# Performance work log

Measured on AMD Instinct MI355X. Metric: run time of the kernel, lower is better.

Reference implementation:

```python
import jax, jax.numpy as jnp
import numpy as np

H_DIM = 1024
NUM_HEADS = 16
HEAD_DIM = H_DIM // NUM_HEADS
EPS = 1e-5


def rms_norm(x, w, eps=EPS):
    var = jnp.mean(jnp.square(x), axis=-1, keepdims=True)
    return x * jax.lax.rsqrt(var + eps) * w


def setup_inputs() -> dict:
    key = jax.random.key(0)
    ks = jax.random.split(key, 8)
    B, S = 2, 2048
    x = jax.random.normal(ks[0], (B, S, H_DIM), dtype=jnp.float32)
    # learned params (orthogonal init approximated by scaled normal for a correctness baseline)
    qkv_w = jax.random.normal(ks[1], (3 * H_DIM, H_DIM), dtype=jnp.float32) / np.sqrt(H_DIM)
    gate_w = jax.random.normal(ks[2], (NUM_HEADS, H_DIM), dtype=jnp.float32) / np.sqrt(H_DIM)
    o_w = jax.random.normal(ks[3], (H_DIM, H_DIM), dtype=jnp.float32) / np.sqrt(H_DIM)
    prenorm_w = jnp.ones((H_DIM,), dtype=jnp.float32)
    q_norm_w = jnp.ones((HEAD_DIM,), dtype=jnp.float32)
    k_norm_w = jnp.ones((HEAD_DIM,), dtype=jnp.float32)
    return {"x": x, "prenorm_w": prenorm_w, "qkv_w": qkv_w, "gate_w": gate_w,
            "o_w": o_w, "q_norm_w": q_norm_w, "k_norm_w": k_norm_w}


def reference(x, prenorm_w, qkv_w, gate_w, o_w, q_norm_w, k_norm_w):
    B, S, D = x.shape
    residual = x
    xn = rms_norm(x, prenorm_w)                                   # [B,S,D]
    qkv = jnp.einsum('bsd,ed->bse', xn, qkv_w)                    # [B,S,3D]
    qkv = qkv.reshape(B, S, 3, NUM_HEADS, HEAD_DIM)
    gate = jnp.einsum('bsd,hd->bsh', xn, gate_w)                  # [B,S,H]
    q, k, v = qkv[:, :, 0], qkv[:, :, 1], qkv[:, :, 2]            # [B,S,H,hd]
    q = rms_norm(q, q_norm_w)
    k = rms_norm(k, k_norm_w)
    scale = 1.0 / np.sqrt(HEAD_DIM).astype(np.float32)
    scores = jnp.einsum('bqhd,bkhd->bhqk', q, k) * scale          # [B,H,S,S]
    attn = jax.nn.softmax(scores, axis=-1)
    out = jnp.einsum('bhqk,bkhd->bhqd', attn, v)                  # [B,H,S,hd]
    out = out * jax.nn.sigmoid(gate).transpose(0, 2, 1)[..., None]
    out = out.transpose(0, 2, 1, 3).reshape(B, S, D)              # [B,S,D]
    return jnp.einsum('bsd,ed->bse', out, o_w) + residual
```

## Files before the change

kernel.cpp:

```cpp
#include <hip/hip_runtime.h>
#include <math.h>

typedef __bf16 bf16x8 __attribute__((ext_vector_type(8)));
typedef float f32x4 __attribute__((ext_vector_type(4)));
typedef float f32x16 __attribute__((ext_vector_type(16)));
typedef unsigned int uint2v __attribute__((ext_vector_type(2)));
typedef unsigned int uint4v __attribute__((ext_vector_type(4)));
typedef unsigned short ushort_t;

#define SEQ 2048
#define MROWS 4096
#define EPS 1e-5f
#define QKS 3200
#define LOG2E 1.4426950408889634f
#define SMAX_B2 17.32f

__device__ __forceinline__ float bf2f(ushort_t u) {
  union { unsigned int i; float f; } c; c.i = ((unsigned int)u) << 16; return c.f;
}
__device__ __forceinline__ ushort_t f2bf(float f) {
  union { unsigned int i; float f; } c; c.f = f;
  unsigned int i = c.i;
  unsigned int r = i + 0x7fffu + ((i >> 16) & 1u);
  return (ushort_t)(r >> 16);
}
__device__ __forceinline__ ushort_t f2bf_fast(float f) {
  union { __bf16 b; ushort_t u; } cv; cv.b = (__bf16)f; return cv.u;
}

__device__ __forceinline__ float exp2_raw(float x) {
  float r; asm("v_exp_f32 %0, %1" : "=v"(r) : "v"(x)); return r;
}

#define CVTPK(d, a, b) asm("v_cvt_pk_bf16_f32 %0, %1, %2" : "=v"(d) : "v"(a), "v"(b))

__device__ __forceinline__ void plane_swap(unsigned int &a, unsigned int &b) {
#if __has_builtin(__builtin_amdgcn_permlane32_swap)
  uint2v r = __builtin_amdgcn_permlane32_swap(a, b, 0, 0);
  a = r.x; b = r.y;
#else
  unsigned int sa = (unsigned int)__shfl_xor((int)a, 32);
  unsigned int sb = (unsigned int)__shfl_xor((int)b, 32);
  int hi = (int)((threadIdx.x & 63) >> 5);
  unsigned int na = hi ? sb : a;
  unsigned int nb = hi ? b : sa;
  a = na; b = nb;
#endif
}

__device__ __forceinline__ void softmax_pack(const f32x16 &stv, float &lp,
                                             uint4v &Fa, uint4v &Fb) {
  float p[16];
  #pragma unroll
  for (int r = 0; r < 16; ++r) p[r] = exp2_raw(stv[r] - SMAX_B2);
  float s0 = (p[0] + p[1]) + (p[2] + p[3]);
  float s1 = (p[4] + p[5]) + (p[6] + p[7]);
  float s2 = (p[8] + p[9]) + (p[10] + p[11]);
  float s3 = (p[12] + p[13]) + (p[14] + p[15]);
  lp += (s0 + s1) + (s2 + s3);
  unsigned int X00, X01, X10, X11, X20, X21, X30, X31;
  CVTPK(X00, p[0], p[1]);   CVTPK(X01, p[2], p[3]);
  CVTPK(X10, p[4], p[5]);   CVTPK(X11, p[6], p[7]);
  CVTPK(X20, p[8], p[9]);   CVTPK(X21, p[10], p[11]);
  CVTPK(X30, p[12], p[13]); CVTPK(X31, p[14], p[15]);
  plane_swap(X00, X10); plane_swap(X01, X11);
  plane_swap(X20, X30); plane_swap(X21, X31);
  Fa.x = X00; Fa.y = X01; Fa.z = X10; Fa.w = X11;
  Fb.x = X20; Fb.y = X21; Fb.z = X30; Fb.w = X31;
}

__device__ __forceinline__ float wave_sum(float v) {
  #pragma unroll
  for (int off = 32; off > 0; off >>= 1) v += __shfl_xor(v, off);
  return v;
}

__global__ void detect_kernel(const unsigned int* __restrict__ xraw, int* __restrict__ flag) {
  int tid = threadIdx.x;
  int cnt = 0;
  for (int i = tid; i < 4096; i += 256) {
    unsigned int e = (xraw[i] >> 7) & 0xFFu;
    cnt += (e >= 100u && e <= 150u) ? 1 : 0;
  }
  __shared__ int sred[256];
  sred[tid] = cnt;
  __syncthreads();
  for (int s = 128; s > 0; s >>= 1) {
    if (tid < s) sred[tid] += sred[tid + s];
    __syncthreads();
  }
  if (tid == 0) flag[0] = (sred[0] > 2048) ? 1 : 0;
}

__global__ void prep_kernel(const void* __restrict__ qkvw_in, const void* __restrict__ gw_in,
                            const void* __restrict__ ow_in, const void* __restrict__ pw_in,
                            const void* __restrict__ qn_in, const void* __restrict__ kn_in,
                            ushort_t* __restrict__ Wcat, ushort_t* __restrict__ ow,
                            float* __restrict__ pwf, float* __restrict__ qnf,
                            float* __restrict__ knf, const int* __restrict__ flag) {
  int bid = blockIdx.x, tid = threadIdx.x;
  int bf = *flag;
  if (bid < 12288) {
    int i = bid * 256 + tid;
    Wcat[i] = bf ? ((const ushort_t*)qkvw_in)[i] : f2bf(((const float*)qkvw_in)[i]);
  } else if (bid < 12352) {
    int i = (bid - 12288) * 256 + tid;
    Wcat[3072 * 1024 + i] = bf ? ((const ushort_t*)gw_in)[i] : f2bf(((const float*)gw_in)[i]);
  } else if (bid < 16448) {
    int i = (bid - 12352) * 256 + tid;
    ow[i] = bf ? ((const ushort_t*)ow_in)[i] : f2bf(((const float*)ow_in)[i]);
  } else {
    for (int i = tid; i < 1024; i += 256)
      pwf[i] = bf ? bf2f(((const ushort_t*)pw_in)[i]) : ((const float*)pw_in)[i];
    if (tid < 64) {
      qnf[tid] = bf ? bf2f(((const ushort_t*)qn_in)[tid]) : ((const float*)qn_in)[tid];
      knf[tid] = bf ? bf2f(((const ushort_t*)kn_in)[tid]) : ((const float*)kn_in)[tid];
    }
  }
}

__global__ void prenorm_kernel(const void* __restrict__ xraw,
                               const float* __restrict__ w,
                               ushort_t* __restrict__ xn,
                               const int* __restrict__ flag) {
  int row = blockIdx.x;
  int tid = threadIdx.x;
  float4 u;
  if (*flag) {
    ushort4 s = ((const ushort4*)xraw)[row * 256 + tid];
    u.x = bf2f(s.x); u.y = bf2f(s.y); u.z = bf2f(s.z); u.w = bf2f(s.w);
  } else {
    u = ((const float4*)xraw)[row * 256 + tid];
  }
  float ss = u.x*u.x + u.y*u.y + u.z*u.z + u.w*u.w;
  ss = wave_sum(ss);
  __shared__ float red[4];
  if ((tid & 63) == 0) red[tid >> 6] = ss;
  __syncthreads();
  float total = red[0] + red[1] + red[2] + red[3];
  float inv = rsqrtf(total * (1.0f / 1024.0f) + EPS);
  float4 wu = ((const float4*)w)[tid];
  ushort4 o;
  o.x = f2bf(u.x * inv * wu.x);
  o.y = f2bf(u.y * inv * wu.y);
  o.z = f2bf(u.z * inv * wu.z);
  o.w = f2bf(u.w * inv * wu.w);
  ((ushort4*)(xn + (long long)row * 1024))[tid] = o;
}

__device__ __forceinline__ void gll16(const ushort_t* g, ushort_t* l) {
  __builtin_amdgcn_global_load_lds(
      (const __attribute__((address_space(1))) unsigned int*)g,
      (__attribute__((address_space(3))) unsigned int*)l, 16, 0, 0);
}

__global__ void gemm_qkv_fused(const ushort_t* __restrict__ A, const ushort_t* __restrict__ B,
                               ushort_t* __restrict__ C, float* __restrict__ gate,
                               const float* __restrict__ qw, const float* __restrict__ kw) {
  __shared__ ushort_t As[128 * 32];
  __shared__ ushort_t Bs[128 * 32];
  int tid = threadIdx.x, wave = tid >> 6, lane = tid & 63;
  int m_blk = blockIdx.y * 128, n_blk = blockIdx.x * 128;
  int wm = (wave & 1) * 64, wn = (wave >> 1) * 64;
  int g = lane >> 4, c = lane & 15;
  int arow = lane >> 2;
  int akc = (lane & 3) << 3;
  f32x4 acc[4][4] = {};
  for (int kt = 0; kt < 1024; kt += 32) {
    #pragma unroll
    for (int i = 0; i < 2; ++i) {
      int rbase = (i * 4 + wave) * 16;
      gll16(A + (long long)(m_blk + rbase + arow) * 1024 + kt + akc, &As[rbase * 32]);
      gll16(B + (long long)(n_blk + rbase + arow) * 1024 + kt + akc, &Bs[rbase * 32]);
    }
    __syncthreads();
    bf16x8 af[4], bfr[4];
    #pragma unroll
    for (int mi = 0; mi < 4; ++mi)
      af[mi] = *(const bf16x8*)&As[(wm + mi * 16 + c) * 32 + (g << 3)];
    #pragma unroll
    for (int ni = 0; ni < 4; ++ni)
      bfr[ni] = *(const bf16x8*)&Bs[(wn + ni * 16 + c) * 32 + (g << 3)];
    #pragma unroll
    for (int mi = 0; mi < 4; ++mi)
      #pragma unroll
      for (int ni = 0; ni < 4; ++ni)
        acc[mi][ni] = __builtin_amdgcn_mfma_f32_16x16x32_bf16(af[mi], bfr[ni], acc[mi][ni], 0, 0, 0);
    __syncthreads();
  }
  int col_base = n_blk + wn;
  if (col_base < 2048) {
    int isk = col_base >= 1024;
    float scale = isk ? 1.0f : (0.125f * LOG2E);
    const float* nw = isk ? kw : qw;
    float w[4];
    #pragma unroll
    for (int ni = 0; ni < 4; ++ni) w[ni] = nw[ni * 16 + c];
    #pragma unroll
    for (int mi = 0; mi < 4; ++mi)
      #pragma unroll
      for (int r = 0; r < 4; ++r) {
        float ss = 0.f;
        #pragma unroll
        for (int ni = 0; ni < 4; ++ni) ss += acc[mi][ni][r] * acc[mi][ni][r];
        #pragma unroll
        for (int off = 8; off > 0; off >>= 1) ss += __shfl_xor(ss, off);
        float inv = rsqrtf(ss * (1.0f / 64.0f) + EPS) * scale;
        int row = m_blk + wm + mi * 16 + g * 4 + r;
        #pragma unroll
        for (int ni = 0; ni < 4; ++ni)
          C[(long long)row * QKS + col_base + ni * 16 + c] = f2bf(acc[mi][ni][r] * inv * w[ni]);
      }
  } else if (col_base < 3072) {
    #pragma unroll
    for (int mi = 0; mi < 4; ++mi)
      #pragma unroll
      for (int r = 0; r < 4; ++r) {
        int row = m_blk + wm + mi * 16 + g * 4 + r;
        #pragma unroll
        for (int ni = 0; ni < 4; ++ni)
          C[(long long)row * QKS + col_base + ni * 16 + c] = f2bf(acc[mi][ni][r]);
      }
  } else if (col_base == 3072) {
    #pragma unroll
    for (int mi = 0; mi < 4; ++mi)
      #pragma unroll
      for (int r = 0; r < 4; ++r) {
        int row = m_blk + wm + mi * 16 + g * 4 + r;
        float v = acc[mi][0][r];
        gate[(long long)row * 16 + c] = 1.0f / (1.0f + __expf(-v));
      }
  }
}

__global__ void gemm_tiled(const ushort_t* __restrict__ A, const ushort_t* __restrict__ B,
                           void* __restrict__ Cv, const void* __restrict__ res,
                           const int* __restrict__ flag,
                           int K, int lda, int ldb, int ldc) {
  __shared__ ushort_t As[128 * 32];
  __shared__ ushort_t Bs[128 * 32];
  int tid = threadIdx.x, wave = tid >> 6, lane = tid & 63;
  int m_blk = blockIdx.y * 128, n_blk = blockIdx.x * 128;
  int wm = (wave & 1) * 64, wn = (wave >> 1) * 64;
  int g = lane >> 4, c = lane & 15;
  int arow = lane >> 2;
  int akc = (lane & 3) << 3;
  f32x4 acc[4][4] = {};
  for (int kt = 0; kt < K; kt += 32) {
    #pragma unroll
    for (int i = 0; i < 2; ++i) {
      int rbase = (i * 4 + wave) * 16;
      gll16(A + (long long)(m_blk + rbase + arow) * lda + kt + akc, &As[rbase * 32]);
      gll16(B + (long long)(n_blk + rbase + arow) * ldb + kt + akc, &Bs[rbase * 32]);
    }
    __syncthreads();
    bf16x8 af[4], bfr[4];
    #pragma unroll
    for (int mi = 0; mi < 4; ++mi)
      af[mi] = *(const bf16x8*)&As[(wm + mi * 16 + c) * 32 + (g << 3)];
    #pragma unroll
    for (int ni = 0; ni < 4; ++ni)
      bfr[ni] = *(const bf16x8*)&Bs[(wn + ni * 16 + c) * 32 + (g << 3)];
    #pragma unroll
    for (int mi = 0; mi < 4; ++mi)
      #pragma unroll
      for (int ni = 0; ni < 4; ++ni)
        acc[mi][ni] = __builtin_amdgcn_mfma_f32_16x16x32_bf16(af[mi], bfr[ni], acc[mi][ni], 0, 0, 0);
    __syncthreads();
  }
  int outbf = flag ? *flag : 1;
  #pragma unroll
  for (int mi = 0; mi < 4; ++mi)
    #pragma unroll
    for (int ni = 0; ni < 4; ++ni)
      #pragma unroll
      for (int r = 0; r < 4; ++r) {
        int row = m_blk + wm + mi * 16 + g * 4 + r;
        int col = n_blk + wn + ni * 16 + c;
        long long idx = (long long)row * ldc + col;
        float v = acc[mi][ni][r];
        if (res) v += outbf ? bf2f(((const ushort_t*)res)[idx]) : ((const float*)res)[idx];
        if (outbf) ((ushort_t*)Cv)[idx] = f2bf(v);
        else       ((float*)Cv)[idx] = v;
      }
}

__global__ void vt_kernel(const ushort_t* __restrict__ qkv, ushort_t* __restrict__ Vt) {
  __shared__ ushort_t tile[64][65];
  int s0 = blockIdx.x * 64;
  int bh = blockIdx.y;
  int b = bh >> 4, h = bh & 15;
  const ushort_t* src = qkv + (long long)b * SEQ * QKS + 2048 + h * 64;
  int d = threadIdx.x & 63, srow = threadIdx.x >> 6;
  #pragma unroll
  for (int i = 0; i < 16; ++i) {
    int sl = i * 4 + srow;
    tile[sl][d] = src[(long long)(s0 + sl) * QKS + d];
  }
  __syncthreads();
  ushort_t* dst = Vt + (long long)bh * 64 * SEQ + s0;
  int sl2 = threadIdx.x & 63, drow = threadIdx.x >> 6;
  #pragma unroll
  for (int i = 0; i < 16; ++i) {
    int dd = i * 4 + drow;
    dst[(long long)dd * SEQ + sl2] = tile[sl2][dd];
  }
}

__global__ void flash_kernel(const ushort_t* __restrict__ qkv, const ushort_t* __restrict__ Vt,
                             const float* __restrict__ gate, ushort_t* __restrict__ ao) {
  __shared__ ushort_t Ks[4][64 * 64];
  __shared__ ushort_t Vs[4][64 * 64];
  int tid = threadIdx.x, wave = tid >> 6, lane = tid & 63;
  int al = lane & 31, hi = lane >> 5;
  int fal = (al & 7) ^ ((al >> 3) & 3);
  int q0 = blockIdx.x * 128;
  int bh = blockIdx.y, b = bh >> 4, h = bh & 15;
  const ushort_t* qbase = qkv + (long long)b * SEQ * QKS + h * 64;
  const ushort_t* kbase = qbase + 1024;
  const ushort_t* vtbase = Vt + (long long)bh * 64 * SEQ;
  int qrow = q0 + wave * 32 + al;
  bf16x8 bq[4];
  #pragma unroll
  for (int dst = 0; dst < 4; ++dst)
    bq[dst] = *(const bf16x8*)(qbase + (long long)qrow * QKS + dst * 16 + hi * 8);
  f32x16 oac0 = {}, oac1 = {};
  float lp = 0.f;
  int srow = lane >> 3;
  int schk = lane & 7;

  #define STAGE(BUF, S0) do {                                                        \
    int gch = ((schk ^ srow ^ wave) & 7) << 3;                                       \
    _Pragma("unroll")                                                                \
    for (int tt = 0; tt < 2; ++tt) {                                                 \
      int rb = tt * 32 + wave * 8;                                                   \
      int row = rb + srow;                                                           \
      gll16(kbase + (long long)((S0) + row) * QKS + gch, &Ks[BUF][rb * 64]);         \
      gll16(vtbase + (long long)row * SEQ + (S0) + gch, &Vs[BUF][rb * 64]);          \
    } } while (0)

  #define PIPE_BAR(N) do {                                                           \
    asm volatile("s_waitcnt vmcnt(" #N ")" ::: "memory");                            \
    __builtin_amdgcn_s_barrier();                                                    \
    asm volatile("" ::: "memory");                                                   \
  } while (0)

  #define COMPUTE(BUF) do {                                                          \
    f32x16 st0 = {}, st1 = {};                                                       \
    __builtin_amdgcn_s_setprio(1);                                                   \
    _Pragma("unroll")                                                                \
    for (int dst = 0; dst < 4; ++dst) {                                              \
      int ph = (((dst << 1) | hi) ^ fal) << 3;                                       \
      bf16x8 ak0 = *(const bf16x8*)&Ks[BUF][al * 64 + ph];                           \
      bf16x8 ak1 = *(const bf16x8*)&Ks[BUF][(32 + al) * 64 + ph];                    \
      st0 = __builtin_amdgcn_mfma_f32_32x32x16_bf16(ak0, bq[dst], st0, 0, 0, 0);     \
      st1 = __builtin_amdgcn_mfma_f32_32x32x16_bf16(ak1, bq[dst], st1, 0, 0, 0);     \
    }                                                                                \
    __builtin_amdgcn_s_setprio(0);                                                   \
    uint4v Fa, Fb, Fc, Fd;                                                           \
    softmax_pack(st0, lp, Fa, Fb);                                                   \
    softmax_pack(st1, lp, Fc, Fd);                                                   \
    bf16x8 pf0 = __builtin_bit_cast(bf16x8, Fa);                                     \
    bf16x8 pf1 = __builtin_bit_cast(bf16x8, Fb);                                     \
    bf16x8 pf2 = __builtin_bit_cast(bf16x8, Fc);                                     \
    bf16x8 pf3 = __builtin_bit_cast(bf16x8, Fd);                                     \
    __builtin_amdgcn_s_setprio(1);                                                   \
    _Pragma("unroll")                                                                \
    for (int kst = 0; kst < 4; ++kst) {                                              \
      int ph = (((kst << 1) | hi) ^ fal) << 3;                                       \
      bf16x8 av0 = *(const bf16x8*)&Vs[BUF][al * 64 + ph];                           \
      bf16x8 av1 = *(const bf16x8*)&Vs[BUF][(32 + al) * 64 + ph];                    \
      bf16x8 pf = (kst == 0) ? pf0 : (kst == 1) ? pf1 : (kst == 2) ? pf2 : pf3;      \
      oac0 = __builtin_amdgcn_mfma_f32_32x32x16_bf16(av0, pf, oac0, 0, 0, 0);        \
      oac1 = __builtin_amdgcn_mfma_f32_32x32x16_bf16(av1, pf, oac1, 0, 0, 0);        \
    }                                                                                \
    __builtin_amdgcn_s_setprio(0);                                                   \
  } while (0)

  STAGE(0, 0);
  STAGE(1, 64);
  for (int it = 0; it < 30; ++it) {
    STAGE((it + 2) & 3, (it + 2) * 64);
    PIPE_BAR(8);
    COMPUTE(it & 3);
  }
  PIPE_BAR(4);
  COMPUTE(2);
  PIPE_BAR(0);
  COMPUTE(3);
  #undef STAGE
  #undef PIPE_BAR
  #undef COMPUTE

  float ltot = lp + __shfl_xor(lp, 32);
  float sg = gate[(long long)(b * SEQ + qrow) * 16 + h];
  float scale = sg / ltot;
  ushort_t* aobase = ao + (long long)(b * SEQ + qrow) * 1024 + h * 64;
  #define OSTORE(OA, MT) do {                                                        \
    _Pragma("unroll")                                                                \
    for (int tt = 0; tt < 4; ++tt) {                                                 \
      ushort4 o;                                                                     \
      o.x = f2bf_fast(OA[4 * tt + 0] * scale);                                       \
      o.y = f2bf_fast(OA[4 * tt + 1] * scale);                                       \
      o.z = f2bf_fast(OA[4 * tt + 2] * scale);                                       \
      o.w = f2bf_fast(OA[4 * tt + 3] * scale);                                       \
      *(ushort4*)(aobase + (MT) * 32 + 8 * tt + 4 * hi) = o;                         \
    } } while (0)
  OSTORE(oac0, 0);
  OSTORE(oac1, 1);
  #undef OSTORE
}

extern "C" void kernel_launch(void* const* d_in, const int* in_sizes, int n_in,
                              void* d_out, int out_size, void* d_ws, size_t ws_size,
                              hipStream_t stream) {
  (void)in_sizes; (void)n_in; (void)out_size; (void)ws_size;
  char* ws = (char*)d_ws;
  ushort_t* Wcat = (ushort_t*)(ws);
  ushort_t* ow   = (ushort_t*)(ws + (7ll << 20));
  float*    pwf  = (float*)   (ws + (9ll << 20));
  float*    qnf  = (float*)   (ws + (9ll << 20) + (8 << 10));
  float*    knf  = (float*)   (ws + (9ll << 20) + (12 << 10));
  int*      flag = (int*)     (ws + (9ll << 20) + (16 << 10));
  float*    gate = (float*)   (ws + (9ll << 20) + (64 << 10));
  ushort_t* xn   = (ushort_t*)(ws + (10ll << 20));
  ushort_t* qkv2 = (ushort_t*)(ws + (18ll << 20));
  ushort_t* Vt   = (ushort_t*)(ws + (44ll << 20));
  ushort_t* ao   = (ushort_t*)(ws + (52ll << 20));

  detect_kernel<<<1, 256, 0, stream>>>((const unsigned int*)d_in[0], flag);
  prep_kernel<<<16449, 256, 0, stream>>>(d_in[2], d_in[3], d_in[4], d_in[1], d_in[5], d_in[6],
                                         Wcat, ow, pwf, qnf, knf, flag);
  prenorm_kernel<<<MROWS, 256, 0, stream>>>(d_in[0], pwf, xn, flag);
  gemm_qkv_fused<<<dim3(25, 32), 256, 0, stream>>>(xn, Wcat, qkv2, gate, qnf, knf);
  vt_kernel<<<dim3(32, 32), 256, 0, stream>>>(qkv2, Vt);
  flash_kernel<<<dim3(16, 32), 256, 0, stream>>>(qkv2, Vt, gate, ao);
  gemm_tiled<<<dim3(8, 32), 256, 0, stream>>>(ao, ow, d_out, d_in[0], flag,
                                              1024, 1024, 1024, 1024);
}
```

Measured before the change: 230.4 us.

## Split flash attention key tiles across wave pairs and remap blocks per XCD

The flash kernel now processes 64 query rows per block instead of 128, and splits each 64-key tile between two wave pairs (each handles 32 keys). Partial outputs and row sums are merged through shared memory at the end. The LDS pipeline shrinks from 4 buffers to 2 (32 KB), with launch bounds allowing 4 blocks per CU, and the 1D grid is remapped so each XCD handles a contiguous set of heads for L2 locality. The intent is more blocks and better occupancy and cache reuse, at the cost of an extra barrier per iteration, a shallower prefetch pipeline, and a cross-wave reduction.

```diff
diff --git a/kernel.cpp b/kernel.cpp
--- a/kernel.cpp
+++ b/kernel.cpp
@@ -307,23 +307,35 @@
   }
 }
 
-__global__ void flash_kernel(const ushort_t* __restrict__ qkv, const ushort_t* __restrict__ Vt,
-                             const float* __restrict__ gate, ushort_t* __restrict__ ao) {
-  __shared__ ushort_t Ks[4][64 * 64];
-  __shared__ ushort_t Vs[4][64 * 64];
+__global__ __launch_bounds__(256, 4)
+void flash_kernel(const ushort_t* __restrict__ qkv, const ushort_t* __restrict__ Vt,
+                  const float* __restrict__ gate, ushort_t* __restrict__ ao) {
+  __shared__ char smem[32768] __attribute__((aligned(16)));
+  ushort_t* KsB = (ushort_t*)smem;
+  ushort_t* VsB = (ushort_t*)(smem + 16384);
   int tid = threadIdx.x, wave = tid >> 6, lane = tid & 63;
   int al = lane & 31, hi = lane >> 5;
   int fal = (al & 7) ^ ((al >> 3) & 3);
-  int q0 = blockIdx.x * 128;
-  int bh = blockIdx.y, b = bh >> 4, h = bh & 15;
+  int qh = wave & 1, kh = wave >> 1;
+  int khb = kh * 32;
+  int bid = blockIdx.x;
+  int xcd = bid & 7, idx = bid >> 3;
+  int bh = (xcd << 2) | (idx >> 5);
+  int q0 = (idx & 31) * 64;
+  int b = bh >> 4, h = bh & 15;
   const ushort_t* qbase = qkv + (long long)b * SEQ * QKS + h * 64;
   const ushort_t* kbase = qbase + 1024;
   const ushort_t* vtbase = Vt + (long long)bh * 64 * SEQ;
-  int qrow = q0 + wave * 32 + al;
+  int qrow = q0 + qh * 32 + al;
   bf16x8 bq[4];
   #pragma unroll
   for (int dst = 0; dst < 4; ++dst)
     bq[dst] = *(const bf16x8*)(qbase + (long long)qrow * QKS + dst * 16 + hi * 8);
+  asm volatile("s_waitcnt vmcnt(0)"
+               :
+               : "v"(__builtin_bit_cast(f32x4, bq[0])), "v"(__builtin_bit_cast(f32x4, bq[1])),
+                 "v"(__builtin_bit_cast(f32x4, bq[2])), "v"(__builtin_bit_cast(f32x4, bq[3]))
+               : "memory");
   f32x16 oac0 = {}, oac1 = {};
   float lp = 0.f;
   int srow = lane >> 3;
@@ -331,12 +343,13 @@
 
   #define STAGE(BUF, S0) do {                                                        \
     int gch = ((schk ^ srow ^ wave) & 7) << 3;                                       \
+    int lbo = (BUF) * 4096;                                                          \
     _Pragma("unroll")                                                                \
     for (int tt = 0; tt < 2; ++tt) {                                                 \
       int rb = tt * 32 + wave * 8;                                                   \
       int row = rb + srow;                                                           \
-      gll16(kbase + (long long)((S0) + row) * QKS + gch, &Ks[BUF][rb * 64]);         \
-      gll16(vtbase + (long long)row * SEQ + (S0) + gch, &Vs[BUF][rb * 64]);          \
+      gll16(kbase + (long long)((S0) + row) * QKS + gch, &KsB[lbo + rb * 64]);       \
+      gll16(vtbase + (long long)row * SEQ + (S0) + gch, &VsB[lbo + rb * 64]);        \
     } } while (0)
 
   #define PIPE_BAR(N) do {                                                           \
@@ -346,31 +359,28 @@
   } while (0)
 
   #define COMPUTE(BUF) do {                                                          \
-    f32x16 st0 = {}, st1 = {};                                                       \
+    int lbo = (BUF) * 4096;                                                          \
+    f32x16 st = {};                                                                  \
     __builtin_amdgcn_s_setprio(1);                                                   \
     _Pragma("unroll")                                                                \
     for (int dst = 0; dst < 4; ++dst) {                                              \
       int ph = (((dst << 1) | hi) ^ fal) << 3;                                       \
-      bf16x8 ak0 = *(const bf16x8*)&Ks[BUF][al * 64 + ph];                           \
-      bf16x8 ak1 = *(const bf16x8*)&Ks[BUF][(32 + al) * 64 + ph];                    \
-      st0 = __builtin_amdgcn_mfma_f32_32x32x16_bf16(ak0, bq[dst], st0, 0, 0, 0);     \
-      st1 = __builtin_amdgcn_mfma_f32_32x32x16_bf16(ak1, bq[dst], st1, 0, 0, 0);     \
+      bf16x8 ak = *(const bf16x8*)&KsB[lbo + (khb + al) * 64 + ph];                  \
+      st = __builtin_amdgcn_mfma_f32_32x32x16_bf16(ak, bq[dst], st, 0, 0, 0);        \
     }                                                                                \
     __builtin_amdgcn_s_setprio(0);                                                   \
-    uint4v Fa, Fb, Fc, Fd;                                                           \
-    softmax_pack(st0, lp, Fa, Fb);                                                   \
-    softmax_pack(st1, lp, Fc, Fd);                                                   \
+    uint4v Fa, Fb;                                                                   \
+    softmax_pack(st, lp, Fa, Fb);                                                    \
     bf16x8 pf0 = __builtin_bit_cast(bf16x8, Fa);                                     \
     bf16x8 pf1 = __builtin_bit_cast(bf16x8, Fb);                                     \
-    bf16x8 pf2 = __builtin_bit_cast(bf16x8, Fc);                                     \
-    bf16x8 pf3 = __builtin_bit_cast(bf16x8, Fd);                                     \
     __builtin_amdgcn_s_setprio(1);                                                   \
     _Pragma("unroll")                                                                \
-    for (int kst = 0; kst < 4; ++kst) {                                              \
-      int ph = (((kst << 1) | hi) ^ fal) << 3;                                       \
-      bf16x8 av0 = *(const bf16x8*)&Vs[BUF][al * 64 + ph];                           \
-      bf16x8 av1 = *(const bf16x8*)&Vs[BUF][(32 + al) * 64 + ph];                    \
-      bf16x8 pf = (kst == 0) ? pf0 : (kst == 1) ? pf1 : (kst == 2) ? pf2 : pf3;      \
+    for (int kst = 0; kst < 2; ++kst) {                                              \
+      int kg = kh * 2 + kst;                                                         \
+      int ph = (((kg << 1) | hi) ^ fal) << 3;                                        \
+      bf16x8 av0 = *(const bf16x8*)&VsB[lbo + al * 64 + ph];                         \
+      bf16x8 av1 = *(const bf16x8*)&VsB[lbo + (32 + al) * 64 + ph];                  \
+      bf16x8 pf = kst ? pf1 : pf0;                                                   \
       oac0 = __builtin_amdgcn_mfma_f32_32x32x16_bf16(av0, pf, oac0, 0, 0, 0);        \
       oac1 = __builtin_amdgcn_mfma_f32_32x32x16_bf16(av1, pf, oac1, 0, 0, 0);        \
     }                                                                                \
@@ -378,37 +388,58 @@
   } while (0)
 
   STAGE(0, 0);
-  STAGE(1, 64);
-  for (int it = 0; it < 30; ++it) {
-    STAGE((it + 2) & 3, (it + 2) * 64);
-    PIPE_BAR(8);
-    COMPUTE(it & 3);
-  }
-  PIPE_BAR(4);
-  COMPUTE(2);
+  for (int it = 0; it < 31; ++it) {
+    STAGE((it + 1) & 1, (it + 1) * 64);
+    PIPE_BAR(4);
+    COMPUTE(it & 1);
+    __builtin_amdgcn_s_barrier();
+  }
   PIPE_BAR(0);
-  COMPUTE(3);
+  COMPUTE(1);
   #undef STAGE
   #undef PIPE_BAR
   #undef COMPUTE
 
   float ltot = lp + __shfl_xor(lp, 32);
-  float sg = gate[(long long)(b * SEQ + qrow) * 16 + h];
-  float scale = sg / ltot;
-  ushort_t* aobase = ao + (long long)(b * SEQ + qrow) * 1024 + h * 64;
-  #define OSTORE(OA, MT) do {                                                        \
-    _Pragma("unroll")                                                                \
-    for (int tt = 0; tt < 4; ++tt) {                                                 \
-      ushort4 o;                                                                     \
-      o.x = f2bf_fast(OA[4 * tt + 0] * scale);                                       \
-      o.y = f2bf_fast(OA[4 * tt + 1] * scale);                                       \
-      o.z = f2bf_fast(OA[4 * tt + 2] * scale);                                       \
-      o.w = f2bf_fast(OA[4 * tt + 3] * scale);                                       \
-      *(ushort4*)(aobase + (MT) * 32 + 8 * tt + 4 * hi) = o;                         \
-    } } while (0)
-  OSTORE(oac0, 0);
-  OSTORE(oac1, 1);
-  #undef OSTORE
+  float* cbuf = (float*)smem;
+  float* lbuf = cbuf + 64 * 65;
+  int qrl = qh * 32 + al;
+  __syncthreads();
+  if (kh == 1) {
+    #pragma unroll
+    for (int r = 0; r < 16; ++r) {
+      int d = (r & 3) + 8 * (r >> 2) + 4 * hi;
+      cbuf[qrl * 65 + d]      = oac0[r];
+      cbuf[qrl * 65 + 32 + d] = oac1[r];
+    }
+    if (hi == 0) lbuf[qrl] = ltot;
+  }
+  __syncthreads();
+  if (kh == 0) {
+    ltot += lbuf[qrl];
+    #pragma unroll
+    for (int r = 0; r < 16; ++r) {
+      int d = (r & 3) + 8 * (r >> 2) + 4 * hi;
+      oac0[r] += cbuf[qrl * 65 + d];
+      oac1[r] += cbuf[qrl * 65 + 32 + d];
+    }
+    float sg = gate[(long long)(b * SEQ + qrow) * 16 + h];
+    float scale = sg / ltot;
+    ushort_t* aobase = ao + (long long)(b * SEQ + qrow) * 1024 + h * 64;
+    #define OSTORE(OA, MT) do {                                                      \
+      _Pragma("unroll")                                                              \
+      for (int tt = 0; tt < 4; ++tt) {                                               \
+        ushort4 o;                                                                   \
+        o.x = f2bf_fast(OA[4 * tt + 0] * scale);                                     \
+        o.y = f2bf_fast(OA[4 * tt + 1] * scale);                                     \
+        o.z = f2bf_fast(OA[4 * tt + 2] * scale);                                     \
+        o.w = f2bf_fast(OA[4 * tt + 3] * scale);                                     \
+        *(ushort4*)(aobase + (MT) * 32 + 8 * tt + 4 * hi) = o;                       \
+      } } while (0)
+    OSTORE(oac0, 0);
+    OSTORE(oac1, 1);
+    #undef OSTORE
+  }
 }
 
 extern "C" void kernel_launch(void* const* d_in, const int* in_sizes, int n_in,
@@ -434,7 +465,7 @@
   prenorm_kernel<<<MROWS, 256, 0, stream>>>(d_in[0], pwf, xn, flag);
   gemm_qkv_fused<<<dim3(25, 32), 256, 0, stream>>>(xn, Wcat, qkv2, gate, qnf, knf);
   vt_kernel<<<dim3(32, 32), 256, 0, stream>>>(qkv2, Vt);
-  flash_kernel<<<dim3(16, 32), 256, 0, stream>>>(qkv2, Vt, gate, ao);
+  flash_kernel<<<dim3(1024), 256, 0, stream>>>(qkv2, Vt, gate, ao);
   gemm_tiled<<<dim3(8, 32), 256, 0, stream>>>(ao, ow, d_out, d_in[0], flag,
                                               1024, 1024, 1024, 1024);
 }
```

After: 230.6 us. About the same (+0.1%).
